# Performance work log

Hardware: AMD Instinct MI355X
Metric: run time of the kernel (lower is better)

Reference implementation:

```python
import jax, jax.numpy as jnp
import numpy as np

B, N, K, D, L = 32, 1024, 16, 256, 256


def setup_inputs() -> dict:
    key = jax.random.key(0)
    k1, k2, k3, k4 = jax.random.split(key, 4)
    targets = jax.random.normal(k1, (B, N, D), dtype=jnp.float32)
    neighbors = jax.random.normal(k2, (B, N, K, D), dtype=jnp.float32)
    a = jax.random.uniform(k3, (B, N, K + 1), dtype=jnp.float32)
    # glorot-uniform-ish kernel
    limit = np.sqrt(6.0 / (D + L)).astype(np.float32)
    kernel = jax.random.uniform(k4, (D, L), dtype=jnp.float32, minval=-limit, maxval=limit)
    return {"targets": targets, "neighbors": neighbors, "a": a, "kernel": kernel}


def reference(targets, neighbors, a, kernel):
    # neighborhood: [B, N, K+1, D] = self node prepended to its K neighbors
    neighborhood = jnp.concatenate([targets[..., None, :], neighbors], axis=-2)
    # matmul with kernel then sum over neighborhood axis (fused via einsum)
    y = jnp.einsum("bnkd,dl->bnl", neighborhood, kernel)  # [B, N, L]
    # degree normalization; guard against isolated nodes (degree ~ 0)
    factor = jnp.sum(a, axis=-1, keepdims=True)  # [B, N, 1]
    factor = jnp.where(factor > 0.5, factor, jnp.ones_like(factor))
    y = y / factor
    # dropout is a no-op at inference; use_bias=False
    return jax.nn.relu(y)
```

## Files before the change

### kernel.cpp

```cpp
#include <hip/hip_runtime.h>


typedef float v4f __attribute__((ext_vector_type(4)));

#define BB 32
#define NN 1024
#define KK 16
#define DD 256
#define LL 256
#define ROWS 32
#define DTILE 16
#define NPASS (DD / DTILE)
#define NTHREADS 256

__device__ __forceinline__ float bcast_lane(float x, int lane) {
    return __int_as_float(__builtin_amdgcn_readlane(__float_as_int(x), lane));
}

__global__ __launch_bounds__(NTHREADS, 4)
void gcn_fused(const float* __restrict__ targets,
               const float* __restrict__ neighbors,
               const float* __restrict__ a,
               const float* __restrict__ kern,
               float* __restrict__ out) {
    __shared__ float kt[2][DTILE * LL];
    __shared__ float invf[ROWS];

    const int t        = threadIdx.x;
    const int w        = t >> 6;
    const int lane     = t & 63;
    const int row_base = blockIdx.x * ROWS;

    const v4f* k4 = (const v4f*)kern;

    v4f stage[4];
    #pragma unroll
    for (int i = 0; i < 4; ++i) stage[i] = k4[i * NTHREADS + t];

    if (t < ROWS) {
        const float* ap = a + (size_t)(row_base + t) * (KK + 1);
        float f = 0.0f;
        #pragma unroll
        for (int j = 0; j < KK + 1; ++j) f += ap[j];
        invf[t] = (f > 0.5f) ? (1.0f / f) : 1.0f;
    }

    const v4f* t4 = (const v4f*)targets;
    const v4f* n4 = (const v4f*)neighbors;
    v4f sreg[8];
    #pragma unroll
    for (int r = 0; r < 8; ++r) {
        const int grow = row_base + w * 8 + r;
        v4f accum = __builtin_nontemporal_load(&t4[(size_t)grow * (DD / 4) + lane]);
        #pragma unroll 4
        for (int k = 0; k < KK; ++k) {
            accum += __builtin_nontemporal_load(
                &n4[((size_t)grow * KK + k) * (DD / 4) + lane]);
        }
        sreg[r] = accum;
    }

    #pragma unroll
    for (int i = 0; i < 4; ++i)
        *(v4f*)&kt[0][(i * NTHREADS + t) * 4] = stage[i];
    __syncthreads();

    v4f acc[8];
    #pragma unroll
    for (int r = 0; r < 8; ++r) acc[r] = v4f{0.0f, 0.0f, 0.0f, 0.0f};

    for (int dt = 0; dt < NPASS; ++dt) {
        const int cur = dt & 1;
        if (dt < NPASS - 1) {
            #pragma unroll
            for (int i = 0; i < 4; ++i)
                stage[i] = k4[(dt + 1) * (DTILE * LL / 4) + i * NTHREADS + t];
        }
        #pragma unroll
        for (int dd = 0; dd < DTILE; ++dd) {
            v4f kv = *(const v4f*)&kt[cur][dd * LL + 4 * lane];
            const int chunk = dt * (DTILE / 4) + (dd >> 2);
            #pragma unroll
            for (int r = 0; r < 8; ++r) {
                const float sv = bcast_lane(sreg[r][dd & 3], chunk);
                acc[r] += sv * kv;
            }
        }
        if (dt < NPASS - 1) {
            *(v4f*)&kt[cur ^ 1][(0 * NTHREADS + t) * 4] = stage[0];
            *(v4f*)&kt[cur ^ 1][(1 * NTHREADS + t) * 4] = stage[1];
            *(v4f*)&kt[cur ^ 1][(2 * NTHREADS + t) * 4] = stage[2];
            *(v4f*)&kt[cur ^ 1][(3 * NTHREADS + t) * 4] = stage[3];
            __syncthreads();
        }
    }

    #pragma unroll
    for (int r = 0; r < 8; ++r) {
        const int rl    = w * 8 + r;
        const float inv = invf[rl];
        v4f v = acc[r] * inv;
        v.x = fmaxf(v.x, 0.0f);
        v.y = fmaxf(v.y, 0.0f);
        v.z = fmaxf(v.z, 0.0f);
        v.w = fmaxf(v.w, 0.0f);
        __builtin_nontemporal_store(v, (v4f*)&out[(size_t)(row_base + rl) * LL + 4 * lane]);
    }
}

extern "C" void kernel_launch(void* const* d_in, const int* in_sizes, int n_in,
                              void* d_out, int out_size, void* d_ws, size_t ws_size,
                              hipStream_t stream) {
    const float* targets   = (const float*)d_in[0];
    const float* neighbors = (const float*)d_in[1];
    const float* a         = (const float*)d_in[2];
    const float* kern      = (const float*)d_in[3];
    float* out = (float*)d_out;
    const int blocks = (BB * NN) / ROWS;
    gcn_fused<<<dim3(blocks), dim3(NTHREADS), 0, stream>>>(targets, neighbors, a, kern, out);
}
```

Measured before the change: 730.7 us.

## Drop LDS kernel staging; read kernel rows directly from global/L2 per wave

Removes the shared-memory double-buffered staging of the weight matrix and its block-wide barriers. Each wave now loads its kernel rows straight from global memory, relying on L2 and cache hits, since every block reads the same 256x256 matrix. The per-row degree normalization is computed per wave in registers and broadcast with readlane, replacing the LDS array. In exchange, each of the four waves fetches the full weight matrix separately, and the loads are no longer prefetched one tile ahead, so global latency may be exposed. The workload is dominated by streaming the neighbors tensor.

After: 746.0 us. 1.02x slower.

```diff
diff --git a/kernel.cpp b/kernel.cpp
--- a/kernel.cpp
+++ b/kernel.cpp
@@ -9,12 +9,12 @@
 #define DD 256
 #define LL 256
 #define ROWS 32
-#define DTILE 16
+#define DTILE 8
 #define NPASS (DD / DTILE)
 #define NTHREADS 256
 
-__device__ __forceinline__ float bcast_lane(float x, int lane) {
-    return __int_as_float(__builtin_amdgcn_readlane(__float_as_int(x), lane));
+__device__ __forceinline__ float bcast(float x, int l) {
+    return __int_as_float(__builtin_amdgcn_readlane(__float_as_int(x), l));
 }
 
 __global__ __launch_bounds__(NTHREADS, 4)
@@ -23,88 +23,66 @@
                const float* __restrict__ a,
                const float* __restrict__ kern,
                float* __restrict__ out) {
-    __shared__ float kt[2][DTILE * LL];
-    __shared__ float invf[ROWS];
-
     const int t        = threadIdx.x;
     const int w        = t >> 6;
     const int lane     = t & 63;
     const int row_base = blockIdx.x * ROWS;
 
-    const v4f* k4 = (const v4f*)kern;
-
-    v4f stage[4];
-    #pragma unroll
-    for (int i = 0; i < 4; ++i) stage[i] = k4[i * NTHREADS + t];
-
-    if (t < ROWS) {
-        const float* ap = a + (size_t)(row_base + t) * (KK + 1);
-        float f = 0.0f;
+    float fsum = 0.0f;
+    {
+        const float* ap = a + (size_t)(row_base + w * 8 + (lane & 7)) * (KK + 1);
         #pragma unroll
-        for (int j = 0; j < KK + 1; ++j) f += ap[j];
-        invf[t] = (f > 0.5f) ? (1.0f / f) : 1.0f;
+        for (int j = 0; j < KK + 1; ++j) fsum += ap[j];
     }
+    const float invf = (fsum > 0.5f) ? (1.0f / fsum) : 1.0f;
 
     const v4f* t4 = (const v4f*)targets;
     const v4f* n4 = (const v4f*)neighbors;
     v4f sreg[8];
     #pragma unroll
     for (int r = 0; r < 8; ++r) {
-        const int grow = row_base + w * 8 + r;
-        v4f accum = __builtin_nontemporal_load(&t4[(size_t)grow * (DD / 4) + lane]);
+        const size_t grow = (size_t)(row_base + w * 8 + r);
+        v4f accum = __builtin_nontemporal_load(&t4[grow * (DD / 4) + lane]);
         #pragma unroll 4
         for (int k = 0; k < KK; ++k) {
             accum += __builtin_nontemporal_load(
-                &n4[((size_t)grow * KK + k) * (DD / 4) + lane]);
+                &n4[(grow * KK + k) * (DD / 4) + lane]);
         }
         sreg[r] = accum;
     }
-
-    #pragma unroll
-    for (int i = 0; i < 4; ++i)
-        *(v4f*)&kt[0][(i * NTHREADS + t) * 4] = stage[i];
-    __syncthreads();
 
     v4f acc[8];
     #pragma unroll
     for (int r = 0; r < 8; ++r) acc[r] = v4f{0.0f, 0.0f, 0.0f, 0.0f};
 
+    const v4f* k4 = (const v4f*)kern;
     for (int dt = 0; dt < NPASS; ++dt) {
-        const int cur = dt & 1;
-        if (dt < NPASS - 1) {
-            #pragma unroll
-            for (int i = 0; i < 4; ++i)
-                stage[i] = k4[(dt + 1) * (DTILE * LL / 4) + i * NTHREADS + t];
-        }
+        v4f kv[DTILE];
+        #pragma unroll
+        for (int dd = 0; dd < DTILE; ++dd)
+            kv[dd] = k4[(size_t)(dt * DTILE + dd) * (LL / 4) + lane];
         #pragma unroll
         for (int dd = 0; dd < DTILE; ++dd) {
-            v4f kv = *(const v4f*)&kt[cur][dd * LL + 4 * lane];
-            const int chunk = dt * (DTILE / 4) + (dd >> 2);
+            const int d     = dt * DTILE + dd;
+            const int chunk = d >> 2;
             #pragma unroll
             for (int r = 0; r < 8; ++r) {
-                const float sv = bcast_lane(sreg[r][dd & 3], chunk);
-                acc[r] += sv * kv;
+                const float sv = bcast(sreg[r][d & 3], chunk);
+                acc[r] += sv * kv[dd];
             }
-        }
-        if (dt < NPASS - 1) {
-            *(v4f*)&kt[cur ^ 1][(0 * NTHREADS + t) * 4] = stage[0];
-            *(v4f*)&kt[cur ^ 1][(1 * NTHREADS + t) * 4] = stage[1];
-            *(v4f*)&kt[cur ^ 1][(2 * NTHREADS + t) * 4] = stage[2];
-            *(v4f*)&kt[cur ^ 1][(3 * NTHREADS + t) * 4] = stage[3];
-            __syncthreads();
         }
     }
 
     #pragma unroll
     for (int r = 0; r < 8; ++r) {
-        const int rl    = w * 8 + r;
-        const float inv = invf[rl];
+        const float inv = bcast(invf, r);
         v4f v = acc[r] * inv;
         v.x = fmaxf(v.x, 0.0f);
         v.y = fmaxf(v.y, 0.0f);
         v.z = fmaxf(v.z, 0.0f);
         v.w = fmaxf(v.w, 0.0f);
-        __builtin_nontemporal_store(v, (v4f*)&out[(size_t)(row_base + rl) * LL + 4 * lane]);
+        __builtin_nontemporal_store(
+            v, (v4f*)&out[(size_t)(row_base + w * 8 + r) * LL + 4 * lane]);
     }
 }
 
```
